# Optimization experiments

Measured on AMD Instinct MI355X. Metric: run time of the kernel, lower is better.

The kernel has to match this reference:

```python
import jax, jax.numpy as jnp
import numpy as np

N0, D, H, E0 = 50000, 128, 128, 800000
N1, E1, A, B, C = 20000, 320000, 100000, 64, 10


def _gcn(x, row, col, ew, n, W, b):
    # GCNConv: out = D^-1/2 (A + I) D^-1/2 (x W) + b, with edge weights
    xw = x @ W
    sl = jnp.arange(n)
    r = jnp.concatenate([row, sl])
    c = jnp.concatenate([col, sl])
    w = jnp.concatenate([ew, jnp.ones((n,), ew.dtype)])
    deg = jax.ops.segment_sum(w, c, num_segments=n)
    dinv = jax.lax.rsqrt(jnp.maximum(deg, 1e-12))
    norm = dinv[r] * w * dinv[c]
    return jax.ops.segment_sum(norm[:, None] * xw[r], c, num_segments=n) + b


def _block(x, row, col, ew, n, W1, b1, W2, b2, Wl, bl):
    # Block with num_inner_layers=2, jumping_knowledge='cat'
    x1 = jax.nn.relu(_gcn(x, row, col, ew, n, W1, b1))
    x2 = jax.nn.relu(_gcn(x1, row, col, ew, n, W2, b2))
    return jnp.concatenate([x1, x2], axis=1) @ Wl + bl


def _seg_max(x, idx, n):
    m = jax.ops.segment_max(x, idx, num_segments=n)
    return jnp.where(jnp.isfinite(m), m, 0.0)  # empty segments -> 0 like scatter_max default


def _lin_init(k, i, o):
    s = 1.0 / np.sqrt(i)
    return jax.random.uniform(k, (i, o), jnp.float32, -s, s)


def setup_inputs() -> dict:
    key = jax.random.key(0)
    ks = jax.random.split(key, 20)
    x = jax.random.normal(ks[0], (N0, D), jnp.float32)
    edge_index0 = jax.random.randint(ks[1], (2, E0), 0, N0)
    edge_weight0 = jax.random.uniform(ks[2], (E0,), jnp.float32)
    batch0 = jnp.sort(jax.random.randint(ks[3], (N0,), 0, B))
    cover_row = jax.random.randint(ks[4], (A,), 0, N0)
    cover_col = jnp.concatenate([jnp.arange(N1), jax.random.randint(ks[5], (A - N1,), 0, N1)])
    edge_index1 = jax.random.randint(ks[6], (2, E1), 0, N1)
    edge_weight1 = jax.random.uniform(ks[7], (E1,), jnp.float32)
    batch1 = jnp.sort(jax.random.randint(ks[8], (N1,), 0, B))
    params = dict(
        w_in1=_lin_init(ks[9], D, H), b_in1=jnp.zeros((H,), jnp.float32),
        w_in2=_lin_init(ks[10], H, H), b_in2=jnp.zeros((H,), jnp.float32),
        w_in_lin=_lin_init(ks[11], 2 * H, H), b_in_lin=jnp.zeros((H,), jnp.float32),
        w_b1=_lin_init(ks[12], 2 * H, H), b_b1=jnp.zeros((H,), jnp.float32),
        w_b2=_lin_init(ks[13], H, H), b_b2=jnp.zeros((H,), jnp.float32),
        w_b_lin=_lin_init(ks[14], 2 * H, H), b_b_lin=jnp.zeros((H,), jnp.float32),
        bn_gamma=jnp.ones((4 * H,), jnp.float32), bn_beta=jnp.zeros((4 * H,), jnp.float32),
        w_l1=_lin_init(ks[15], 4 * H, H), b_l1=jnp.zeros((H,), jnp.float32),
        w_l2=_lin_init(ks[16], H, C), b_l2=jnp.zeros((C,), jnp.float32),
    )
    return dict(x=x, edge_index0=edge_index0, edge_weight0=edge_weight0, batch0=batch0,
                cover_row=cover_row, cover_col=cover_col, edge_index1=edge_index1,
                edge_weight1=edge_weight1, batch1=batch1, **params)


def reference(x, edge_index0, edge_weight0, batch0, cover_row, cover_col,
              edge_index1, edge_weight1, batch1,
              w_in1, b_in1, w_in2, b_in2, w_in_lin, b_in_lin,
              w_b1, b_b1, w_b2, b_b2, w_b_lin, b_b_lin,
              bn_gamma, bn_beta, w_l1, b_l1, w_l2, b_l2):
    r0, c0 = edge_index0[0], edge_index0[1]
    h = jax.nn.relu(_block(x, r0, c0, edge_weight0, N0, w_in1, b_in1, w_in2, b_in2, w_in_lin, b_in_lin))
    xs = [jax.ops.segment_sum(h, batch0, num_segments=B), _seg_max(h, batch0, B)]
    # cover_pool_node: add + max over k-plex cover assignments
    hg = h[cover_row]
    h2 = jnp.concatenate([jax.ops.segment_sum(hg, cover_col, num_segments=N1),
                          _seg_max(hg, cover_col, N1)], axis=1)
    r1, c1 = edge_index1[0], edge_index1[1]
    h2 = jax.nn.relu(_block(h2, r1, c1, edge_weight1, N1, w_b1, b_b1, w_b2, b_b2, w_b_lin, b_b_lin))
    xs.append(jax.ops.segment_sum(h2, batch1, num_segments=B))
    xs.append(_seg_max(h2, batch1, B))
    z = jnp.concatenate(xs, axis=1)  # [B, 4H]
    # BatchNorm1d in eval mode: running stats (mean=0, var=1), eps=1e-5
    z = z * (bn_gamma * jax.lax.rsqrt(jnp.asarray(1.0 + 1e-5, z.dtype))) + bn_beta
    z = jax.nn.relu(z @ w_l1 + b_l1)
    logits = z @ w_l2 + b_l2  # dropout skipped (eval mode)
    return jax.nn.softmax(logits, axis=-1)
```

## Files before the change

kernel.cpp:

```cpp
#include <hip/hip_runtime.h>
#include <cmath>

#define HF 128
#define EPB 2048

namespace {

typedef __attribute__((ext_vector_type(8))) short short8;
typedef __attribute__((ext_vector_type(4))) float f32x4;

inline int cdiv(int a, int b) { return (a + b - 1) / b; }

__device__ inline unsigned short f2bf(float x) {
    unsigned u = __float_as_uint(x);
    return (unsigned short)((u + 0x7fffu + ((u >> 16) & 1u)) >> 16);
}
__device__ inline float bf2f(unsigned short u) {
    return __uint_as_float((unsigned)u << 16);
}
__device__ inline float bflo(unsigned v) { return __uint_as_float(v << 16); }
__device__ inline float bfhi(unsigned v) { return __uint_as_float(v & 0xffff0000u); }

#define FIXS 4194304.0f
#define FIXINV 2.384185791015625e-07f
#define SUMMASK ((1ULL << 40) - 1)

template <int K, bool AF32>
__device__ __forceinline__ void gemm_dev(int bid, const void* __restrict__ A1v, int lda1,
                                         const void* __restrict__ A2v, int lda2,
                                         const unsigned short* __restrict__ wpk,
                                         const float* __restrict__ bias, int relu,
                                         unsigned short* __restrict__ out, int N) {
    const int t = threadIdx.x;
    const int wv = t >> 6, lane = t & 63;
    const int l15 = lane & 15, lhi = lane >> 4;
    const int rbase = bid * 128 + wv * 32;

    f32x4 acc[2][8];
#pragma unroll
    for (int i = 0; i < 2; ++i)
#pragma unroll
        for (int g = 0; g < 8; ++g) acc[i][g] = {0.f, 0.f, 0.f, 0.f};

    int r[2];
#pragma unroll
    for (int ri = 0; ri < 2; ++ri) {
        int rr = rbase + ri * 16 + l15;
        r[ri] = (rr < N) ? rr : (N - 1);
    }

    for (int kc = 0; kc < K / 32; ++kc) {
        int kb = kc * 32 + lhi * 8;
        short8 a[2];
#pragma unroll
        for (int ri = 0; ri < 2; ++ri) {
            if (AF32) {
                const float* A = (const float*)A1v;
                const float* p = A + (size_t)r[ri] * lda1 + kb;
                float4 f0 = *reinterpret_cast<const float4*>(p);
                float4 f1 = *reinterpret_cast<const float4*>(p + 4);
                a[ri][0] = (short)f2bf(f0.x); a[ri][1] = (short)f2bf(f0.y);
                a[ri][2] = (short)f2bf(f0.z); a[ri][3] = (short)f2bf(f0.w);
                a[ri][4] = (short)f2bf(f1.x); a[ri][5] = (short)f2bf(f1.y);
                a[ri][6] = (short)f2bf(f1.z); a[ri][7] = (short)f2bf(f1.w);
            } else {
                const unsigned short* base;
                int kk, ld;
                if (K == 256 && kb >= 128) { base = (const unsigned short*)A2v; kk = kb - 128; ld = lda2; }
                else                       { base = (const unsigned short*)A1v; kk = kb;       ld = lda1; }
                a[ri] = *reinterpret_cast<const short8*>(base + (size_t)r[ri] * ld + kk);
            }
        }
        const unsigned short* wb = wpk + (size_t)(kc * 8) * 512 + lane * 8;
#pragma unroll
        for (int g = 0; g < 8; ++g) {
            short8 b = *reinterpret_cast<const short8*>(wb + (size_t)g * 512);
            acc[0][g] = __builtin_amdgcn_mfma_f32_16x16x32_bf16(a[0], b, acc[0][g], 0, 0, 0);
            acc[1][g] = __builtin_amdgcn_mfma_f32_16x16x32_bf16(a[1], b, acc[1][g], 0, 0, 0);
        }
    }

#pragma unroll
    for (int ri = 0; ri < 2; ++ri) {
#pragma unroll
        for (int g = 0; g < 8; ++g) {
            int col = l15 + g * 16;
            float bb = bias ? bias[col] : 0.f;
#pragma unroll
            for (int e = 0; e < 4; ++e) {
                int rr = rbase + ri * 16 + lhi * 4 + e;
                if (rr < N) {
                    float v = acc[ri][g][e] + bb;
                    if (relu) v = fmaxf(v, 0.f);
                    out[(size_t)rr * 128 + col] = f2bf(v);
                }
            }
        }
    }
}

template <int K, bool AF32>
__global__ void k_mfma_gemm(const void* __restrict__ A1v, int lda1,
                            const void* __restrict__ A2v, int lda2,
                            const unsigned short* __restrict__ wpk,
                            const float* __restrict__ bias, int relu,
                            unsigned short* __restrict__ out, int N) {
    gemm_dev<K, AF32>(blockIdx.x, A1v, lda1, A2v, lda2, wpk, bias, relu, out, N);
}

__device__ __forceinline__ void hist_dev(int e, int E, const int* __restrict__ col,
                                         const float* __restrict__ ew,
                                         unsigned long long* __restrict__ dc,
                                         unsigned* __restrict__ rank) {
    if (e < E) {
        unsigned long long v = (1ULL << 40) | (unsigned long long)(ew[e] * FIXS + 0.5f);
        unsigned long long old = atomicAdd(&dc[col[e]], v);
        rank[e] = (unsigned)(old >> 40);
    }
}

__device__ inline void scan256(int* s, int v, int gid, int n, int* __restrict__ excl,
                               int* __restrict__ partial, int pb) {
    s[threadIdx.x] = v;
    __syncthreads();
    for (int off = 1; off < 256; off <<= 1) {
        int t = (threadIdx.x >= off) ? s[threadIdx.x - off] : 0;
        __syncthreads();
        s[threadIdx.x] += t;
        __syncthreads();
    }
    if (gid < n) excl[gid] = s[threadIdx.x] - v;
    if (threadIdx.x == 255) partial[pb] = s[255];
}

__device__ __forceinline__ void fill_dev(int b, int t, const int* __restrict__ row,
                                         const int* __restrict__ col, const float* __restrict__ ew,
                                         const unsigned* __restrict__ rank,
                                         const float* __restrict__ dinv, const int* __restrict__ rp,
                                         int2* __restrict__ ed, int E, int Nn) {
    int xcd = b & 7, chunk = b >> 3;
    int lo = (int)((long long)Nn * xcd >> 3), hi = (int)((long long)Nn * (xcd + 1) >> 3);
    int base = chunk * EPB;
#pragma unroll
    for (int i = 0; i < EPB; i += 256) {
        int e = base + i + t;
        if (e < E) {
            int c = col[e];
            if (c >= lo && c < hi) {
                int r = row[e];
                ed[rp[c] + rank[e]] = make_int2(r, __float_as_int(ew[e] * dinv[r] * dinv[c]));
            }
        }
    }
}

__device__ __forceinline__ void gather_dev(int b, const unsigned* __restrict__ xw, int n,
                                           const int* __restrict__ rp, const int2* __restrict__ ed,
                                           const float* __restrict__ dinv,
                                           const float* __restrict__ bias,
                                           unsigned* __restrict__ out) {
    int wid = (b * 256 + (int)threadIdx.x) >> 6;
    if (wid >= n) return;
    int lane = threadIdx.x & 63;
    int s = rp[wid], e = rp[wid + 1];
    float d = dinv[wid];
    unsigned v = xw[(size_t)wid * 64 + lane];
    float ax = bflo(v) * d * d, ay = bfhi(v) * d * d;
    float bx = 0.f, by = 0.f, cx = 0.f, cy = 0.f, dx = 0.f, dy = 0.f;
    int i = s;
    for (; i + 4 <= e; i += 4) {
        unsigned long long p0 = __builtin_nontemporal_load((const unsigned long long*)(ed + i));
        unsigned long long p1 = __builtin_nontemporal_load((const unsigned long long*)(ed + i + 1));
        unsigned long long p2 = __builtin_nontemporal_load((const unsigned long long*)(ed + i + 2));
        unsigned long long p3 = __builtin_nontemporal_load((const unsigned long long*)(ed + i + 3));
        unsigned v0 = xw[(size_t)(unsigned)(p0 & 0xffffffffu) * 64 + lane];
        unsigned v1 = xw[(size_t)(unsigned)(p1 & 0xffffffffu) * 64 + lane];
        unsigned v2 = xw[(size_t)(unsigned)(p2 & 0xffffffffu) * 64 + lane];
        unsigned v3 = xw[(size_t)(unsigned)(p3 & 0xffffffffu) * 64 + lane];
        float c0 = __uint_as_float((unsigned)(p0 >> 32));
        float c1 = __uint_as_float((unsigned)(p1 >> 32));
        float c2 = __uint_as_float((unsigned)(p2 >> 32));
        float c3 = __uint_as_float((unsigned)(p3 >> 32));
        ax += c0 * bflo(v0); ay += c0 * bfhi(v0);
        bx += c1 * bflo(v1); by += c1 * bfhi(v1);
        cx += c2 * bflo(v2); cy += c2 * bfhi(v2);
        dx += c3 * bflo(v3); dy += c3 * bfhi(v3);
    }
    for (; i < e; ++i) {
        unsigned long long p0 = __builtin_nontemporal_load((const unsigned long long*)(ed + i));
        unsigned v0 = xw[(size_t)(unsigned)(p0 & 0xffffffffu) * 64 + lane];
        float c0 = __uint_as_float((unsigned)(p0 >> 32));
        ax += c0 * bflo(v0); ay += c0 * bfhi(v0);
    }
    ax += bx + cx + dx;
    ay += by + cy + dy;
    float2 bb = *reinterpret_cast<const float2*>(bias + lane * 2);
    ax = fmaxf(ax + bb.x, 0.f);
    ay = fmaxf(ay + bb.y, 0.f);
    out[(size_t)wid * 64 + lane] = (unsigned)f2bf(ax) | ((unsigned)f2bf(ay) << 16);
}

__global__ void k_prep0(const float* __restrict__ w0, const float* __restrict__ w1,
                        const float* __restrict__ w2, const float* __restrict__ w3,
                        const float* __restrict__ w4, const float* __restrict__ w5,
                        unsigned short* __restrict__ wpk,
                        const int* __restrict__ b0, int n0, const int* __restrict__ b1,
                        int n1, int B, int* __restrict__ bst0, int* __restrict__ bst1) {
    int b = blockIdx.x, t = threadIdx.x;
    if (b < 576) {
        int idx = b * 256 + t;
        const float* src; int local;
        if      (idx < 16384)  { src = w0; local = idx; }
        else if (idx < 32768)  { src = w1; local = idx - 16384; }
        else if (idx < 65536)  { src = w2; local = idx - 32768; }
        else if (idx < 98304)  { src = w3; local = idx - 65536; }
        else if (idx < 114688) { src = w4; local = idx - 98304; }
        else                   { src = w5; local = idx - 114688; }
        int e = local & 7, lane = (local >> 3) & 63, g = (local >> 9) & 7, kc = local >> 12;
        int colw = (lane & 15) + 16 * g;
        int k = kc * 32 + ((lane >> 4) << 3) + e;
        wpk[idx] = f2bf(src[k * 128 + colw]);
        return;
    }
    int idx = t;
    if (idx < 2 * (B + 1)) {
        int which = idx > B;
        int bb = which ? idx - (B + 1) : idx;
        const int* arr = which ? b1 : b0;
        int lo = 0, hi = which ? n1 : n0;
        while (lo < hi) {
            int mid = (lo + hi) >> 1;
            if (arr[mid] < bb) lo = mid + 1; else hi = mid;
        }
        (which ? bst1 : bst0)[bb] = lo;
    }
}

__global__ void k_prep1(const float* __restrict__ x, const unsigned short* __restrict__ wpk,
                        unsigned short* __restrict__ xw, int N0gemm, int nbG,
                        const int* __restrict__ col0, const float* __restrict__ ew0,
                        unsigned long long* __restrict__ dc0, unsigned* __restrict__ rank0,
                        int E0) {
    int b = blockIdx.x;
    if (b < nbG) {
        gemm_dev<128, true>(b, x, 128, nullptr, 0, wpk, nullptr, 0, xw, N0gemm);
        return;
    }
    b -= nbG;
    hist_dev(b * 256 + (int)threadIdx.x, E0, col0, ew0, dc0, rank0);
}

__global__ void k_scanA(const unsigned long long* __restrict__ dc0, int* __restrict__ rp0,
                        int* __restrict__ part0, float* __restrict__ dinv0, int n0) {
    __shared__ int s[256];
    int gid = blockIdx.x * 256 + threadIdx.x;
    int v = (gid < n0) ? (int)(dc0[gid] >> 40) : 0;
    scan256(s, v, gid, n0, rp0, part0, blockIdx.x);
    if (gid < n0) dinv0[gid] = rsqrtf(1.0f + (float)(dc0[gid] & SUMMASK) * FIXINV);
}

__global__ void k_scan2a(int* __restrict__ p0, int nb0) {
    __shared__ int s[256];
    int v = (threadIdx.x < nb0) ? p0[threadIdx.x] : 0;
    s[threadIdx.x] = v;
    __syncthreads();
    for (int off = 1; off < 256; off <<= 1) {
        int t = (threadIdx.x >= off) ? s[threadIdx.x - off] : 0;
        __syncthreads();
        s[threadIdx.x] += t;
        __syncthreads();
    }
    if (threadIdx.x < nb0) p0[threadIdx.x] = s[threadIdx.x] - v;
}

__global__ void k_scan3a(int* __restrict__ rp0, const int* __restrict__ part0, int n0, int tot) {
    int gid = blockIdx.x * 256 + threadIdx.x;
    if (gid < n0) rp0[gid] += part0[blockIdx.x];
    if (gid == 0) rp0[n0] = tot;
}

__global__ void k_fill0(const int* __restrict__ row0, const int* __restrict__ col0,
                        const float* __restrict__ ew0, const unsigned* __restrict__ rank0,
                        const float* __restrict__ dinv0, const int* __restrict__ rp0,
                        int2* __restrict__ ed0, int E0, int N0n) {
    fill_dev(blockIdx.x, threadIdx.x, row0, col0, ew0, rank0, dinv0, rp0, ed0, E0, N0n);
}

__global__ void k_gather_hist(const unsigned* __restrict__ xw, int n,
                              const int* __restrict__ rp, const int2* __restrict__ ed,
                              const float* __restrict__ dinv, const float* __restrict__ bias,
                              unsigned* __restrict__ out, int G,
                              const int* __restrict__ col1, const float* __restrict__ ew1,
                              unsigned long long* __restrict__ dc1, unsigned* __restrict__ rank1,
                              int E1, int nb1,
                              const int* __restrict__ ccol, int* __restrict__ ccnt,
                              unsigned* __restrict__ rankc, int A) {
    int b = blockIdx.x;
    if (b < G) { gather_dev(b, xw, n, rp, ed, dinv, bias, out); return; }
    b -= G;
    int t = threadIdx.x;
    if (b < nb1) { hist_dev(b * 256 + t, E1, col1, ew1, dc1, rank1); return; }
    b -= nb1;
    int e = b * 256 + t;
    if (e < A) rankc[e] = (unsigned)atomicAdd(&ccnt[ccol[e]], 1);
}

__global__ void k_gemm_scan(const void* __restrict__ A1v, const unsigned short* __restrict__ wpk,
                            unsigned short* __restrict__ out, int N, int nbG,
                            const unsigned long long* __restrict__ dc1, int* __restrict__ rp1,
                            int* __restrict__ part1, float* __restrict__ dinv1, int n1, int nbs1,
                            const int* __restrict__ ccnt, int* __restrict__ crp,
                            int* __restrict__ cpart, int nc) {
    __shared__ int s[256];
    int b = blockIdx.x;
    if (b < nbG) {
        gemm_dev<128, false>(b, A1v, 128, nullptr, 0, wpk, nullptr, 0, out, N);
        return;
    }
    b -= nbG;
    if (b < nbs1) {
        int gid = b * 256 + threadIdx.x;
        int v = (gid < n1) ? (int)(dc1[gid] >> 40) : 0;
        scan256(s, v, gid, n1, rp1, part1, b);
        if (gid < n1) dinv1[gid] = rsqrtf(1.0f + (float)(dc1[gid] & SUMMASK) * FIXINV);
        return;
    }
    b -= nbs1;
    {
        int gid = b * 256 + threadIdx.x;
        int v = (gid < nc) ? ccnt[gid] : 0;
        scan256(s, v, gid, nc, crp, cpart, b);
    }
}

__global__ void k_scan2b(int* __restrict__ p1, int nb1, int* __restrict__ p2, int nb2) {
    __shared__ int s[256];
    int* p = (blockIdx.x == 0) ? p1 : p2;
    int nb = (blockIdx.x == 0) ? nb1 : nb2;
    int v = (threadIdx.x < nb) ? p[threadIdx.x] : 0;
    s[threadIdx.x] = v;
    __syncthreads();
    for (int off = 1; off < 256; off <<= 1) {
        int t = (threadIdx.x >= off) ? s[threadIdx.x - off] : 0;
        __syncthreads();
        s[threadIdx.x] += t;
        __syncthreads();
    }
    if (threadIdx.x < nb) p[threadIdx.x] = s[threadIdx.x] - v;
}

__global__ void k_scan3b(int* __restrict__ rp1, const int* __restrict__ part1, int n1, int tot1,
                         int nb1, int* __restrict__ crp, const int* __restrict__ cpart,
                         int nc, int totc) {
    int b = blockIdx.x, t = threadIdx.x;
    if (b < nb1) {
        int gid = b * 256 + t;
        if (gid < n1) rp1[gid] += part1[b];
        if (gid == 0) rp1[n1] = tot1;
        return;
    }
    b -= nb1;
    int gid = b * 256 + t;
    if (gid < nc) crp[gid] += cpart[b];
    if (gid == 0) crp[nc] = totc;
}

__global__ void k_gather_fill(const unsigned* __restrict__ xw, int n,
                              const int* __restrict__ rp, const int2* __restrict__ ed,
                              const float* __restrict__ dinv, const float* __restrict__ bias,
                              unsigned* __restrict__ out, int G,
                              const int* __restrict__ row1, const int* __restrict__ col1,
                              const float* __restrict__ ew1, const unsigned* __restrict__ rank1,
                              const float* __restrict__ dinv1, const int* __restrict__ rp1,
                              int2* __restrict__ ed1, int E1, int N1n, int g1b,
                              const int* __restrict__ crow, const int* __restrict__ ccol,
                              const unsigned* __restrict__ rankc, const int* __restrict__ crp,
                              int* __restrict__ csrcs, int A) {
    int b = blockIdx.x, t = threadIdx.x;
    if (b < G) { gather_dev(b, xw, n, rp, ed, dinv, bias, out); return; }
    b -= G;
    if (b < g1b) { fill_dev(b, t, row1, col1, ew1, rank1, dinv1, rp1, ed1, E1, N1n); return; }
    b -= g1b;
    {
        int xcd = b & 7, chunk = b >> 3;
        int lo = (int)((long long)N1n * xcd >> 3), hi = (int)((long long)N1n * (xcd + 1) >> 3);
        int base = chunk * EPB;
#pragma unroll
        for (int i = 0; i < EPB; i += 256) {
            int e = base + i + t;
            if (e < A) {
                int c = ccol[e];
                if (c >= lo && c < hi) csrcs[crp[c] + rankc[e]] = crow[e];
            }
        }
    }
}

__global__ void k_gather(const unsigned* __restrict__ xw, int n, const int* __restrict__ rp,
                         const int2* __restrict__ ed, const float* __restrict__ dinv,
                         const float* __restrict__ bias, unsigned* __restrict__ out) {
    gather_dev(blockIdx.x, xw, n, rp, ed, dinv, bias, out);
}

__global__ void k_pool_cover(const unsigned short* __restrict__ h, const int* __restrict__ bst,
                             float* __restrict__ psum, float* __restrict__ pmax, int nsplit,
                             int nbpool, const unsigned* __restrict__ h32,
                             const int* __restrict__ crp, const int* __restrict__ csrcs,
                             unsigned* __restrict__ h2, int n1) {
    int t = threadIdx.x;
    if ((int)blockIdx.x < nbpool) {
        int blk = blockIdx.x;
        int b = blk / nsplit, sub = (blk % nsplit) * 2 + (t >> 7);
        int col = t & 127;
        int r0 = bst[b], r1 = bst[b + 1];
        float sum = 0.f, mx = 0.f;
        for (int r = r0 + sub; r < r1; r += 2 * nsplit) {
            float v = bf2f(h[(size_t)r * HF + col]);
            sum += v;
            mx = fmaxf(mx, v);
        }
        atomicAdd(&psum[b * HF + col], sum);
        atomicMax(reinterpret_cast<int*>(&pmax[b * HF + col]), __float_as_int(mx));
        return;
    }
    int wid = (((int)blockIdx.x - nbpool) * 256 + t) >> 6;
    if (wid >= n1) return;
    int lane = t & 63;
    int s = crp[wid], e = crp[wid + 1];
    float sx = 0.f, sy = 0.f, mx = 0.f, my = 0.f;
    for (int i = s; i < e; ++i) {
        unsigned v = h32[(size_t)csrcs[i] * 64 + lane];
        float vx = bflo(v), vy = bfhi(v);
        sx += vx; sy += vy;
        mx = fmaxf(mx, vx); my = fmaxf(my, vy);
    }
    h2[(size_t)wid * 128 + lane]      = (unsigned)f2bf(sx) | ((unsigned)f2bf(sy) << 16);
    h2[(size_t)wid * 128 + 64 + lane] = (unsigned)f2bf(mx) | ((unsigned)f2bf(my) << 16);
}

__global__ void k_pool256(const unsigned short* __restrict__ h, const int* __restrict__ bst,
                          float* __restrict__ psum, float* __restrict__ pmax, int nsplit) {
    int t = threadIdx.x;
    int blk = blockIdx.x;
    int b = blk / nsplit, sub = (blk % nsplit) * 2 + (t >> 7);
    int col = t & 127;
    int r0 = bst[b], r1 = bst[b + 1];
    float sum = 0.f, mx = 0.f;
    for (int r = r0 + sub; r < r1; r += 2 * nsplit) {
        float v = bf2f(h[(size_t)r * HF + col]);
        sum += v;
        mx = fmaxf(mx, v);
    }
    atomicAdd(&psum[b * HF + col], sum);
    atomicMax(reinterpret_cast<int*>(&pmax[b * HF + col]), __float_as_int(mx));
}

__global__ void k_head(const float* __restrict__ p0s, const float* __restrict__ p0m,
                       const float* __restrict__ p1s, const float* __restrict__ p1m,
                       const float* __restrict__ gamma, const float* __restrict__ beta,
                       const float* __restrict__ w1, const float* __restrict__ b1,
                       const float* __restrict__ w2, const float* __restrict__ b2,
                       float* __restrict__ out) {
    __shared__ float z[512];
    __shared__ float z1[128];
    __shared__ float lg[10];
    int b = blockIdx.x, t = threadIdx.x;
    const float s = rsqrtf(1.0f + 1e-5f);
    z[t]       = p0s[b * 128 + t] * (gamma[t] * s)       + beta[t];
    z[128 + t] = p0m[b * 128 + t] * (gamma[128 + t] * s) + beta[128 + t];
    z[256 + t] = p1s[b * 128 + t] * (gamma[256 + t] * s) + beta[256 + t];
    z[384 + t] = p1m[b * 128 + t] * (gamma[384 + t] * s) + beta[384 + t];
    __syncthreads();
    float acc = b1[t];
    for (int k = 0; k < 512; ++k) acc += z[k] * w1[k * 128 + t];
    z1[t] = fmaxf(acc, 0.f);
    __syncthreads();
    if (t < 10) {
        float a2 = b2[t];
        for (int k = 0; k < 128; ++k) a2 += z1[k] * w2[k * 10 + t];
        lg[t] = a2;
    }
    __syncthreads();
    if (t == 0) {
        float m = lg[0];
        for (int c = 1; c < 10; ++c) m = fmaxf(m, lg[c]);
        float e[10], ssum = 0.f;
        for (int c = 0; c < 10; ++c) { e[c] = expf(lg[c] - m); ssum += e[c]; }
        for (int c = 0; c < 10; ++c) out[b * 10 + c] = e[c] / ssum;
    }
}

}

extern "C" void kernel_launch(void* const* d_in, const int* in_sizes, int n_in,
                              void* d_out, int out_size, void* d_ws, size_t ws_size,
                              hipStream_t stream) {
    const float* x      = (const float*)d_in[0];
    const int*   ei0    = (const int*)d_in[1];
    const float* ew0    = (const float*)d_in[2];
    const int*   batch0 = (const int*)d_in[3];
    const int*   crow   = (const int*)d_in[4];
    const int*   ccol   = (const int*)d_in[5];
    const int*   ei1    = (const int*)d_in[6];
    const float* ew1    = (const float*)d_in[7];
    const int*   batch1 = (const int*)d_in[8];
    const float* w_in1  = (const float*)d_in[9];
    const float* b_in1  = (const float*)d_in[10];
    const float* w_in2  = (const float*)d_in[11];
    const float* b_in2  = (const float*)d_in[12];
    const float* w_inl  = (const float*)d_in[13];
    const float* b_inl  = (const float*)d_in[14];
    const float* w_b1   = (const float*)d_in[15];
    const float* b_b1   = (const float*)d_in[16];
    const float* w_b2   = (const float*)d_in[17];
    const float* b_b2   = (const float*)d_in[18];
    const float* w_bl   = (const float*)d_in[19];
    const float* b_bl   = (const float*)d_in[20];
    const float* gamma  = (const float*)d_in[21];
    const float* beta   = (const float*)d_in[22];
    const float* w_l1   = (const float*)d_in[23];
    const float* b_l1   = (const float*)d_in[24];
    const float* w_l2   = (const float*)d_in[25];
    const float* b_l2   = (const float*)d_in[26];

    const int N0 = in_sizes[0] / 128;
    const int E0 = in_sizes[2];
    const int A  = in_sizes[4];
    const int E1 = in_sizes[7];
    const int N1 = in_sizes[8];
    const int B  = out_size / 10;

    const int* row0 = ei0;
    const int* col0 = ei0 + E0;
    const int* row1 = ei1;
    const int* col1 = ei1 + E1;

    char* wsp = (char*)d_ws;
    size_t off = 0;
    auto alloc = [&](size_t bytes) -> char* {
        char* p = wsp + off;
        off += (bytes + 255) & ~(size_t)255;
        return p;
    };
    unsigned long long* dc0 = (unsigned long long*)alloc((size_t)N0 * 8);
    unsigned long long* dc1 = (unsigned long long*)alloc((size_t)N1 * 8);
    int*   ccnt  = (int*)alloc((size_t)N1 * 4);
    float* p0s   = (float*)alloc((size_t)B * HF * 4 * 4);
    float* p0m   = p0s + (size_t)B * HF;
    float* p1s   = p0m + (size_t)B * HF;
    float* p1m   = p1s + (size_t)B * HF;
    size_t zero_bytes = off;

    unsigned* xw  = (unsigned*)alloc((size_t)N0 * 64 * 4);
    unsigned* x1  = (unsigned*)alloc((size_t)N0 * 64 * 4);
    unsigned* x2  = (unsigned*)alloc((size_t)N0 * 64 * 4);
    unsigned* h   = (unsigned*)alloc((size_t)N0 * 64 * 4);
    unsigned* h2  = (unsigned*)alloc((size_t)N1 * 128 * 4);
    unsigned short* wpk = (unsigned short*)alloc(147456 * 2);
    float* dinv0 = (float*)alloc((size_t)N0 * 4);
    float* dinv1 = (float*)alloc((size_t)N1 * 4);
    int*   rp0   = (int*)alloc(((size_t)N0 + 1) * 4);
    int*   rp1   = (int*)alloc(((size_t)N1 + 1) * 4);
    int*   crp   = (int*)alloc(((size_t)N1 + 1) * 4);
    int*   part0 = (int*)alloc(256 * 4);
    int*   part1 = (int*)alloc(256 * 4);
    int*   cpart = (int*)alloc(256 * 4);
    int2*  ed0   = (int2*)alloc((size_t)E0 * 8);
    int2*  ed1   = (int2*)alloc((size_t)E1 * 8);
    int*   csrcs = (int*)alloc((size_t)A * 4);
    unsigned* rank0 = (unsigned*)alloc((size_t)E0 * 4);
    unsigned* rank1 = (unsigned*)alloc((size_t)E1 * 4);
    unsigned* rankc = (unsigned*)alloc((size_t)A * 4);
    int*   bst0  = (int*)alloc((size_t)(B + 1) * 4);
    int*   bst1  = (int*)alloc((size_t)(B + 1) * 4);
    (void)ws_size; (void)n_in;

    const int NSPLIT = 16;
    const int nbG0 = cdiv(N0, 128), nbG1 = cdiv(N1, 128);
    const int nbE0 = cdiv(E0, 256), nbE1 = cdiv(E1, 256), nbC = cdiv(A, 256);
    const int nbs0 = cdiv(N0, 256), nbs1 = cdiv(N1, 256), nbsc = cdiv(N1, 256);
    const int g1f = cdiv(E1, EPB) * 8, gcf = cdiv(A, EPB) * 8, g0f = cdiv(E0, EPB) * 8;
    const int G0 = cdiv(N0, 4), G1 = cdiv(N1, 4);

    hipMemsetAsync(dc0, 0, zero_bytes, stream);

    k_prep0<<<577, 256, 0, stream>>>(w_in1, w_in2, w_inl, w_b1, w_b2, w_bl, wpk,
                                     batch0, N0, batch1, N1, B, bst0, bst1);

    k_prep1<<<nbG0 + nbE0, 256, 0, stream>>>(x, wpk, (unsigned short*)xw, N0, nbG0,
                                             col0, ew0, dc0, rank0, E0);

    k_scanA<<<nbs0, 256, 0, stream>>>(dc0, rp0, part0, dinv0, N0);
    k_scan2a<<<1, 256, 0, stream>>>(part0, nbs0);
    k_scan3a<<<nbs0, 256, 0, stream>>>(rp0, part0, N0, E0);
    k_fill0<<<g0f, 256, 0, stream>>>(row0, col0, ew0, rank0, dinv0, rp0, ed0, E0, N0);

    k_gather_hist<<<G0 + nbE1 + nbC, 256, 0, stream>>>(
        xw, N0, rp0, ed0, dinv0, b_in1, x1, G0,
        col1, ew1, dc1, rank1, E1, nbE1, ccol, ccnt, rankc, A);

    k_gemm_scan<<<nbG0 + nbs1 + nbsc, 256, 0, stream>>>(
        x1, wpk + 16384, (unsigned short*)xw, N0, nbG0,
        dc1, rp1, part1, dinv1, N1, nbs1, ccnt, crp, cpart, N1);

    k_scan2b<<<2, 256, 0, stream>>>(part1, nbs1, cpart, nbsc);
    k_scan3b<<<nbs1 + nbsc, 256, 0, stream>>>(rp1, part1, N1, E1, nbs1, crp, cpart, N1, A);

    k_gather_fill<<<G0 + g1f + gcf, 256, 0, stream>>>(
        xw, N0, rp0, ed0, dinv0, b_in2, x2, G0,
        row1, col1, ew1, rank1, dinv1, rp1, ed1, E1, N1, g1f,
        crow, ccol, rankc, crp, csrcs, A);

    k_mfma_gemm<256, false><<<nbG0, 256, 0, stream>>>(
        x1, 128, (const unsigned short*)x2, 128, wpk + 32768, b_inl, 1,
        (unsigned short*)h, N0);

    k_pool_cover<<<B * NSPLIT + cdiv(N1, 4), 256, 0, stream>>>(
        (const unsigned short*)h, bst0, p0s, p0m, NSPLIT, B * NSPLIT,
        h, crp, csrcs, h2, N1);

    k_mfma_gemm<256, false><<<nbG1, 256, 0, stream>>>(
        h2, 256, (const unsigned short*)h2 + 128, 256, wpk + 65536, nullptr, 0,
        (unsigned short*)xw, N1);
    k_gather<<<G1, 256, 0, stream>>>(xw, N1, rp1, ed1, dinv1, b_b1, x1);
    k_mfma_gemm<128, false><<<nbG1, 256, 0, stream>>>(
        x1, 128, nullptr, 0, wpk + 98304, nullptr, 0, (unsigned short*)xw, N1);
    k_gather<<<G1, 256, 0, stream>>>(xw, N1, rp1, ed1, dinv1, b_b2, x2);
    k_mfma_gemm<256, false><<<nbG1, 256, 0, stream>>>(
        x1, 128, (const unsigned short*)x2, 128, wpk + 114688, b_bl, 1,
        (unsigned short*)h, N1);

    k_pool256<<<B * NSPLIT, 256, 0, stream>>>((const unsigned short*)h, bst1, p1s, p1m, NSPLIT);

    k_head<<<B, 128, 0, stream>>>(p0s, p0m, p1s, p1m, gamma, beta, w_l1, b_l1, w_l2, b_l2,
                                  (float*)d_out);
}
```

Measured before the change: 397.6 us.

## Bucket CSR edges by source-row chunk to improve gather locality

Splits each destination node's CSR segment into sub-buckets keyed by the source row's 8192-node chunk, so edges within each row are ordered by source region and gathered feature rows are more clustered in cache. The histogram, scans (now 8 elements per thread) and fill use the composite key, and dinv is computed by summing across sub-buckets. The gather loop also switches from nontemporal 8-byte loads to aligned 16-byte edge loads with an alignment prologue. The cost is larger count and offset arrays, more scan work, and extra memset bytes.

```diff
diff --git a/kernel.cpp b/kernel.cpp
--- a/kernel.cpp
+++ b/kernel.cpp
@@ -3,11 +3,13 @@
 
 #define HF 128
 #define EPB 2048
+#define CSH 13
 
 namespace {
 
 typedef __attribute__((ext_vector_type(8))) short short8;
 typedef __attribute__((ext_vector_type(4))) float f32x4;
+typedef unsigned long long u64;
 
 inline int cdiv(int a, int b) { return (a + b - 1) / b; }
 
@@ -108,36 +110,45 @@
     gemm_dev<K, AF32>(blockIdx.x, A1v, lda1, A2v, lda2, wpk, bias, relu, out, N);
 }
 
-__device__ __forceinline__ void hist_dev(int e, int E, const int* __restrict__ col,
-                                         const float* __restrict__ ew,
-                                         unsigned long long* __restrict__ dc,
-                                         unsigned* __restrict__ rank) {
+__device__ __forceinline__ void hist_dev(int e, int E, const int* __restrict__ row,
+                                         const int* __restrict__ col,
+                                         const float* __restrict__ ew, int NC,
+                                         u64* __restrict__ dc, unsigned* __restrict__ rank) {
     if (e < E) {
-        unsigned long long v = (1ULL << 40) | (unsigned long long)(ew[e] * FIXS + 0.5f);
-        unsigned long long old = atomicAdd(&dc[col[e]], v);
+        int key = col[e] * NC + (row[e] >> CSH);
+        u64 v = (1ULL << 40) | (u64)(ew[e] * FIXS + 0.5f);
+        u64 old = atomicAdd(&dc[key], v);
         rank[e] = (unsigned)(old >> 40);
     }
 }
 
-__device__ inline void scan256(int* s, int v, int gid, int n, int* __restrict__ excl,
-                               int* __restrict__ partial, int pb) {
-    s[threadIdx.x] = v;
+__device__ __forceinline__ void scanBig(int* s, const int* v8, int tsum, int b, int n2,
+                                        int* __restrict__ rp, int* __restrict__ part) {
+    int t = threadIdx.x;
+    s[t] = tsum;
     __syncthreads();
     for (int off = 1; off < 256; off <<= 1) {
-        int t = (threadIdx.x >= off) ? s[threadIdx.x - off] : 0;
+        int tv = (t >= off) ? s[t - off] : 0;
         __syncthreads();
-        s[threadIdx.x] += t;
+        s[t] += tv;
         __syncthreads();
     }
-    if (gid < n) excl[gid] = s[threadIdx.x] - v;
-    if (threadIdx.x == 255) partial[pb] = s[255];
+    int excl = s[t] - tsum;
+    int g0 = b * 2048 + t * 8;
+#pragma unroll
+    for (int j = 0; j < 8; ++j) {
+        int g = g0 + j;
+        if (g < n2) rp[g] = excl;
+        excl += v8[j];
+    }
+    if (t == 255) part[b] = s[255];
 }
 
 __device__ __forceinline__ void fill_dev(int b, int t, const int* __restrict__ row,
                                          const int* __restrict__ col, const float* __restrict__ ew,
                                          const unsigned* __restrict__ rank,
-                                         const float* __restrict__ dinv, const int* __restrict__ rp,
-                                         int2* __restrict__ ed, int E, int Nn) {
+                                         const float* __restrict__ dinv, const int* __restrict__ rp2,
+                                         int NC, int2* __restrict__ ed, int E, int Nn) {
     int xcd = b & 7, chunk = b >> 3;
     int lo = (int)((long long)Nn * xcd >> 3), hi = (int)((long long)Nn * (xcd + 1) >> 3);
     int base = chunk * EPB;
@@ -148,48 +159,52 @@
             int c = col[e];
             if (c >= lo && c < hi) {
                 int r = row[e];
-                ed[rp[c] + rank[e]] = make_int2(r, __float_as_int(ew[e] * dinv[r] * dinv[c]));
+                int key = c * NC + (r >> CSH);
+                ed[rp2[key] + rank[e]] = make_int2(r, __float_as_int(ew[e] * dinv[r] * dinv[c]));
             }
         }
     }
 }
 
-__device__ __forceinline__ void gather_dev(int b, const unsigned* __restrict__ xw, int n,
-                                           const int* __restrict__ rp, const int2* __restrict__ ed,
+__device__ __forceinline__ void gather_dev(int b, const unsigned* __restrict__ xw, int n, int NC,
+                                           const int* __restrict__ rp2, const int2* __restrict__ ed,
                                            const float* __restrict__ dinv,
                                            const float* __restrict__ bias,
                                            unsigned* __restrict__ out) {
     int wid = (b * 256 + (int)threadIdx.x) >> 6;
     if (wid >= n) return;
     int lane = threadIdx.x & 63;
-    int s = rp[wid], e = rp[wid + 1];
+    int s = rp2[(size_t)wid * NC], e = rp2[(size_t)wid * NC + NC];
     float d = dinv[wid];
     unsigned v = xw[(size_t)wid * 64 + lane];
     float ax = bflo(v) * d * d, ay = bfhi(v) * d * d;
     float bx = 0.f, by = 0.f, cx = 0.f, cy = 0.f, dx = 0.f, dy = 0.f;
     int i = s;
+    if ((i & 1) && i < e) {
+        int2 e0 = ed[i];
+        unsigned v0 = xw[(size_t)e0.x * 64 + lane];
+        float c0 = __int_as_float(e0.y);
+        ax += c0 * bflo(v0); ay += c0 * bfhi(v0);
+        ++i;
+    }
     for (; i + 4 <= e; i += 4) {
-        unsigned long long p0 = __builtin_nontemporal_load((const unsigned long long*)(ed + i));
-        unsigned long long p1 = __builtin_nontemporal_load((const unsigned long long*)(ed + i + 1));
-        unsigned long long p2 = __builtin_nontemporal_load((const unsigned long long*)(ed + i + 2));
-        unsigned long long p3 = __builtin_nontemporal_load((const unsigned long long*)(ed + i + 3));
-        unsigned v0 = xw[(size_t)(unsigned)(p0 & 0xffffffffu) * 64 + lane];
-        unsigned v1 = xw[(size_t)(unsigned)(p1 & 0xffffffffu) * 64 + lane];
-        unsigned v2 = xw[(size_t)(unsigned)(p2 & 0xffffffffu) * 64 + lane];
-        unsigned v3 = xw[(size_t)(unsigned)(p3 & 0xffffffffu) * 64 + lane];
-        float c0 = __uint_as_float((unsigned)(p0 >> 32));
-        float c1 = __uint_as_float((unsigned)(p1 >> 32));
-        float c2 = __uint_as_float((unsigned)(p2 >> 32));
-        float c3 = __uint_as_float((unsigned)(p3 >> 32));
+        int4 q0 = *reinterpret_cast<const int4*>(ed + i);
+        int4 q1 = *reinterpret_cast<const int4*>(ed + i + 2);
+        unsigned v0 = xw[(size_t)q0.x * 64 + lane];
+        unsigned v1 = xw[(size_t)q0.z * 64 + lane];
+        unsigned v2 = xw[(size_t)q1.x * 64 + lane];
+        unsigned v3 = xw[(size_t)q1.z * 64 + lane];
+        float c0 = __int_as_float(q0.y), c1 = __int_as_float(q0.w);
+        float c2 = __int_as_float(q1.y), c3 = __int_as_float(q1.w);
         ax += c0 * bflo(v0); ay += c0 * bfhi(v0);
         bx += c1 * bflo(v1); by += c1 * bfhi(v1);
         cx += c2 * bflo(v2); cy += c2 * bfhi(v2);
         dx += c3 * bflo(v3); dy += c3 * bfhi(v3);
     }
     for (; i < e; ++i) {
-        unsigned long long p0 = __builtin_nontemporal_load((const unsigned long long*)(ed + i));
-        unsigned v0 = xw[(size_t)(unsigned)(p0 & 0xffffffffu) * 64 + lane];
-        float c0 = __uint_as_float((unsigned)(p0 >> 32));
+        int2 e0 = ed[i];
+        unsigned v0 = xw[(size_t)e0.x * 64 + lane];
+        float c0 = __int_as_float(e0.y);
         ax += c0 * bflo(v0); ay += c0 * bfhi(v0);
     }
     ax += bx + cx + dx;
@@ -238,25 +253,41 @@
 
 __global__ void k_prep1(const float* __restrict__ x, const unsigned short* __restrict__ wpk,
                         unsigned short* __restrict__ xw, int N0gemm, int nbG,
-                        const int* __restrict__ col0, const float* __restrict__ ew0,
-                        unsigned long long* __restrict__ dc0, unsigned* __restrict__ rank0,
-                        int E0) {
+                        const int* __restrict__ row0, const int* __restrict__ col0,
+                        const float* __restrict__ ew0, int NC0,
+                        u64* __restrict__ dc0, unsigned* __restrict__ rank0, int E0) {
     int b = blockIdx.x;
     if (b < nbG) {
         gemm_dev<128, true>(b, x, 128, nullptr, 0, wpk, nullptr, 0, xw, N0gemm);
         return;
     }
     b -= nbG;
-    hist_dev(b * 256 + (int)threadIdx.x, E0, col0, ew0, dc0, rank0);
-}
-
-__global__ void k_scanA(const unsigned long long* __restrict__ dc0, int* __restrict__ rp0,
-                        int* __restrict__ part0, float* __restrict__ dinv0, int n0) {
+    hist_dev(b * 256 + (int)threadIdx.x, E0, row0, col0, ew0, NC0, dc0, rank0);
+}
+
+__global__ void k_scanA(const u64* __restrict__ dc0, int* __restrict__ rp2, int* __restrict__ part,
+                        float* __restrict__ dinv0, int n2, int nbs, int NC, int n0) {
     __shared__ int s[256];
-    int gid = blockIdx.x * 256 + threadIdx.x;
-    int v = (gid < n0) ? (int)(dc0[gid] >> 40) : 0;
-    scan256(s, v, gid, n0, rp0, part0, blockIdx.x);
-    if (gid < n0) dinv0[gid] = rsqrtf(1.0f + (float)(dc0[gid] & SUMMASK) * FIXINV);
+    int b = blockIdx.x, t = threadIdx.x;
+    if (b < nbs) {
+        int g0 = b * 2048 + t * 8;
+        int v8[8]; int tsum = 0;
+#pragma unroll
+        for (int j = 0; j < 8; ++j) {
+            int g = g0 + j;
+            v8[j] = (g < n2) ? (int)(dc0[g] >> 40) : 0;
+            tsum += v8[j];
+        }
+        scanBig(s, v8, tsum, b, n2, rp2, part);
+        return;
+    }
+    b -= nbs;
+    int i = b * 256 + t;
+    if (i < n0) {
+        u64 acc = 0;
+        for (int c = 0; c < NC; ++c) acc += dc0[(size_t)i * NC + c] & SUMMASK;
+        dinv0[i] = rsqrtf(1.0f + (float)acc * FIXINV);
+    }
 }
 
 __global__ void k_scan2a(int* __restrict__ p0, int nb0) {
@@ -273,63 +304,96 @@
     if (threadIdx.x < nb0) p0[threadIdx.x] = s[threadIdx.x] - v;
 }
 
-__global__ void k_scan3a(int* __restrict__ rp0, const int* __restrict__ part0, int n0, int tot) {
-    int gid = blockIdx.x * 256 + threadIdx.x;
-    if (gid < n0) rp0[gid] += part0[blockIdx.x];
-    if (gid == 0) rp0[n0] = tot;
+__global__ void k_scan3a(int* __restrict__ rp2, const int* __restrict__ part, int n2, int tot) {
+    int b = blockIdx.x, t = threadIdx.x;
+    int g0 = b * 2048 + t * 8;
+    int p = part[b];
+#pragma unroll
+    for (int j = 0; j < 8; ++j) {
+        int g = g0 + j;
+        if (g < n2) rp2[g] += p;
+    }
+    if (g0 == 0) rp2[n2] = tot;
 }
 
 __global__ void k_fill0(const int* __restrict__ row0, const int* __restrict__ col0,
                         const float* __restrict__ ew0, const unsigned* __restrict__ rank0,
-                        const float* __restrict__ dinv0, const int* __restrict__ rp0,
+                        const float* __restrict__ dinv0, const int* __restrict__ rp2, int NC0,
                         int2* __restrict__ ed0, int E0, int N0n) {
-    fill_dev(blockIdx.x, threadIdx.x, row0, col0, ew0, rank0, dinv0, rp0, ed0, E0, N0n);
-}
-
-__global__ void k_gather_hist(const unsigned* __restrict__ xw, int n,
-                              const int* __restrict__ rp, const int2* __restrict__ ed,
+    fill_dev(blockIdx.x, threadIdx.x, row0, col0, ew0, rank0, dinv0, rp2, NC0, ed0, E0, N0n);
+}
+
+__global__ void k_gather_hist(const unsigned* __restrict__ xw, int n, int NC,
+                              const int* __restrict__ rp2, const int2* __restrict__ ed,
                               const float* __restrict__ dinv, const float* __restrict__ bias,
                               unsigned* __restrict__ out, int G,
-                              const int* __restrict__ col1, const float* __restrict__ ew1,
-                              unsigned long long* __restrict__ dc1, unsigned* __restrict__ rank1,
+                              const int* __restrict__ row1, const int* __restrict__ col1,
+                              const float* __restrict__ ew1, int NC1,
+                              u64* __restrict__ dc1, unsigned* __restrict__ rank1,
                               int E1, int nb1,
-                              const int* __restrict__ ccol, int* __restrict__ ccnt,
-                              unsigned* __restrict__ rankc, int A) {
+                              const int* __restrict__ crow, const int* __restrict__ ccol,
+                              int NCC, int* __restrict__ ccnt2, unsigned* __restrict__ rankc,
+                              int A) {
     int b = blockIdx.x;
-    if (b < G) { gather_dev(b, xw, n, rp, ed, dinv, bias, out); return; }
+    if (b < G) { gather_dev(b, xw, n, NC, rp2, ed, dinv, bias, out); return; }
     b -= G;
     int t = threadIdx.x;
-    if (b < nb1) { hist_dev(b * 256 + t, E1, col1, ew1, dc1, rank1); return; }
+    if (b < nb1) { hist_dev(b * 256 + t, E1, row1, col1, ew1, NC1, dc1, rank1); return; }
     b -= nb1;
     int e = b * 256 + t;
-    if (e < A) rankc[e] = (unsigned)atomicAdd(&ccnt[ccol[e]], 1);
+    if (e < A) {
+        int key = ccol[e] * NCC + (crow[e] >> CSH);
+        rankc[e] = (unsigned)atomicAdd(&ccnt2[key], 1);
+    }
 }
 
 __global__ void k_gemm_scan(const void* __restrict__ A1v, const unsigned short* __restrict__ wpk,
                             unsigned short* __restrict__ out, int N, int nbG,
-                            const unsigned long long* __restrict__ dc1, int* __restrict__ rp1,
-                            int* __restrict__ part1, float* __restrict__ dinv1, int n1, int nbs1,
-                            const int* __restrict__ ccnt, int* __restrict__ crp,
-                            int* __restrict__ cpart, int nc) {
+                            const u64* __restrict__ dc1, int* __restrict__ rp1,
+                            int* __restrict__ part1, int n21, int nbs1,
+                            float* __restrict__ dinv1, int NC1, int n1, int nbd1,
+                            const int* __restrict__ ccnt2, int* __restrict__ crp2,
+                            int* __restrict__ cpart, int n2c) {
     __shared__ int s[256];
-    int b = blockIdx.x;
+    int b = blockIdx.x, t = threadIdx.x;
     if (b < nbG) {
         gemm_dev<128, false>(b, A1v, 128, nullptr, 0, wpk, nullptr, 0, out, N);
         return;
     }
     b -= nbG;
     if (b < nbs1) {
-        int gid = b * 256 + threadIdx.x;
-        int v = (gid < n1) ? (int)(dc1[gid] >> 40) : 0;
-        scan256(s, v, gid, n1, rp1, part1, b);
-        if (gid < n1) dinv1[gid] = rsqrtf(1.0f + (float)(dc1[gid] & SUMMASK) * FIXINV);
+        int g0 = b * 2048 + t * 8;
+        int v8[8]; int tsum = 0;
+#pragma unroll
+        for (int j = 0; j < 8; ++j) {
+            int g = g0 + j;
+            v8[j] = (g < n21) ? (int)(dc1[g] >> 40) : 0;
+            tsum += v8[j];
+        }
+        scanBig(s, v8, tsum, b, n21, rp1, part1);
         return;
     }
     b -= nbs1;
+    if (b < nbd1) {
+        int i = b * 256 + t;
+        if (i < n1) {
+            u64 acc = 0;
+            for (int c = 0; c < NC1; ++c) acc += dc1[(size_t)i * NC1 + c] & SUMMASK;
+            dinv1[i] = rsqrtf(1.0f + (float)acc * FIXINV);
+        }
+        return;
+    }
+    b -= nbd1;
     {
-        int gid = b * 256 + threadIdx.x;
-        int v = (gid < nc) ? ccnt[gid] : 0;
-        scan256(s, v, gid, nc, crp, cpart, b);
+        int g0 = b * 2048 + t * 8;
+        int v8[8]; int tsum = 0;
+#pragma unroll
+        for (int j = 0; j < 8; ++j) {
+            int g = g0 + j;
+            v8[j] = (g < n2c) ? ccnt2[g] : 0;
+            tsum += v8[j];
+        }
+        scanBig(s, v8, tsum, b, n2c, crp2, cpart);
     }
 }
 
@@ -349,37 +413,52 @@
     if (threadIdx.x < nb) p[threadIdx.x] = s[threadIdx.x] - v;
 }
 
-__global__ void k_scan3b(int* __restrict__ rp1, const int* __restrict__ part1, int n1, int tot1,
-                         int nb1, int* __restrict__ crp, const int* __restrict__ cpart,
-                         int nc, int totc) {
+__global__ void k_scan3b(int* __restrict__ rp1, const int* __restrict__ part1, int n21, int tot1,
+                         int nb1, int* __restrict__ crp2, const int* __restrict__ cpart,
+                         int n2c, int totc) {
     int b = blockIdx.x, t = threadIdx.x;
     if (b < nb1) {
-        int gid = b * 256 + t;
-        if (gid < n1) rp1[gid] += part1[b];
-        if (gid == 0) rp1[n1] = tot1;
+        int g0 = b * 2048 + t * 8;
+        int p = part1[b];
+#pragma unroll
+        for (int j = 0; j < 8; ++j) {
+            int g = g0 + j;
+            if (g < n21) rp1[g] += p;
+        }
+        if (g0 == 0) rp1[n21] = tot1;
         return;
     }
     b -= nb1;
-    int gid = b * 256 + t;
-    if (gid < nc) crp[gid] += cpart[b];
-    if (gid == 0) crp[nc] = totc;
-}
-
-__global__ void k_gather_fill(const unsigned* __restrict__ xw, int n,
-                              const int* __restrict__ rp, const int2* __restrict__ ed,
+    {
+        int g0 = b * 2048 + t * 8;
+        int p = cpart[b];
+#pragma unroll
+        for (int j = 0; j < 8; ++j) {
+            int g = g0 + j;
+            if (g < n2c) crp2[g] += p;
+        }
+        if (g0 == 0) crp2[n2c] = totc;
+    }
+}
+
+__global__ void k_gather_fill(const unsigned* __restrict__ xw, int n, int NC,
+                              const int* __restrict__ rp2, const int2* __restrict__ ed,
                               const float* __restrict__ dinv, const float* __restrict__ bias,
                               unsigned* __restrict__ out, int G,
                               const int* __restrict__ row1, const int* __restrict__ col1,
                               const float* __restrict__ ew1, const unsigned* __restrict__ rank1,
                               const float* __restrict__ dinv1, const int* __restrict__ rp1,
-                              int2* __restrict__ ed1, int E1, int N1n, int g1b,
+                              int NC1, int2* __restrict__ ed1, int E1, int N1n, int g1b,
                               const int* __restrict__ crow, const int* __restrict__ ccol,
-                              const unsigned* __restrict__ rankc, const int* __restrict__ crp,
-                              int* __restrict__ csrcs, int A) {
+                              const unsigned* __restrict__ rankc, const int* __restrict__ crp2,
+                              int NCC, int* __restrict__ csrcs, int A) {
     int b = blockIdx.x, t = threadIdx.x;
-    if (b < G) { gather_dev(b, xw, n, rp, ed, dinv, bias, out); return; }
+    if (b < G) { gather_dev(b, xw, n, NC, rp2, ed, dinv, bias, out); return; }
     b -= G;
-    if (b < g1b) { fill_dev(b, t, row1, col1, ew1, rank1, dinv1, rp1, ed1, E1, N1n); return; }
+    if (b < g1b) {
+        fill_dev(b, t, row1, col1, ew1, rank1, dinv1, rp1, NC1, ed1, E1, N1n);
+        return;
+    }
     b -= g1b;
     {
         int xcd = b & 7, chunk = b >> 3;
@@ -390,23 +469,27 @@
             int e = base + i + t;
             if (e < A) {
                 int c = ccol[e];
-                if (c >= lo && c < hi) csrcs[crp[c] + rankc[e]] = crow[e];
+                if (c >= lo && c < hi) {
+                    int r = crow[e];
+                    csrcs[crp2[c * NCC + (r >> CSH)] + rankc[e]] = r;
+                }
             }
         }
     }
 }
 
-__global__ void k_gather(const unsigned* __restrict__ xw, int n, const int* __restrict__ rp,
-                         const int2* __restrict__ ed, const float* __restrict__ dinv,
-                         const float* __restrict__ bias, unsigned* __restrict__ out) {
-    gather_dev(blockIdx.x, xw, n, rp, ed, dinv, bias, out);
+__global__ void k_gather(const unsigned* __restrict__ xw, int n, int NC,
+                         const int* __restrict__ rp2, const int2* __restrict__ ed,
+                         const float* __restrict__ dinv, const float* __restrict__ bias,
+                         unsigned* __restrict__ out) {
+    gather_dev(blockIdx.x, xw, n, NC, rp2, ed, dinv, bias, out);
 }
 
 __global__ void k_pool_cover(const unsigned short* __restrict__ h, const int* __restrict__ bst,
                              float* __restrict__ psum, float* __restrict__ pmax, int nsplit,
                              int nbpool, const unsigned* __restrict__ h32,
-                             const int* __restrict__ crp, const int* __restrict__ csrcs,
-                             unsigned* __restrict__ h2, int n1) {
+                             const int* __restrict__ crp2, int NCC,
+                             const int* __restrict__ csrcs, unsigned* __restrict__ h2, int n1) {
     int t = threadIdx.x;
     if ((int)blockIdx.x < nbpool) {
         int blk = blockIdx.x;
@@ -426,7 +509,7 @@
     int wid = (((int)blockIdx.x - nbpool) * 256 + t) >> 6;
     if (wid >= n1) return;
     int lane = t & 63;
-    int s = crp[wid], e = crp[wid + 1];
+    int s = crp2[(size_t)wid * NCC], e = crp2[(size_t)wid * NCC + NCC];
     float sx = 0.f, sy = 0.f, mx = 0.f, my = 0.f;
     for (int i = s; i < e; ++i) {
         unsigned v = h32[(size_t)csrcs[i] * 64 + lane];
@@ -535,6 +618,11 @@
     const int* row1 = ei1;
     const int* col1 = ei1 + E1;
 
+    const int NC0 = cdiv(N0, 1 << CSH);
+    const int NC1 = cdiv(N1, 1 << CSH);
+    const int NCC = NC0;
+    const int n2_0 = N0 * NC0, n2_1 = N1 * NC1, n2_c = N1 * NCC;
+
     char* wsp = (char*)d_ws;
     size_t off = 0;
     auto alloc = [&](size_t bytes) -> char* {
@@ -542,13 +630,13 @@
         off += (bytes + 255) & ~(size_t)255;
         return p;
     };
-    unsigned long long* dc0 = (unsigned long long*)alloc((size_t)N0 * 8);
-    unsigned long long* dc1 = (unsigned long long*)alloc((size_t)N1 * 8);
-    int*   ccnt  = (int*)alloc((size_t)N1 * 4);
-    float* p0s   = (float*)alloc((size_t)B * HF * 4 * 4);
-    float* p0m   = p0s + (size_t)B * HF;
-    float* p1s   = p0m + (size_t)B * HF;
-    float* p1m   = p1s + (size_t)B * HF;
+    u64*  dc0   = (u64*)alloc((size_t)n2_0 * 8);
+    u64*  dc1   = (u64*)alloc((size_t)n2_1 * 8);
+    int*  ccnt2 = (int*)alloc((size_t)n2_c * 4);
+    float* p0s  = (float*)alloc((size_t)B * HF * 4 * 4);
+    float* p0m  = p0s + (size_t)B * HF;
+    float* p1s  = p0m + (size_t)B * HF;
+    float* p1m  = p1s + (size_t)B * HF;
     size_t zero_bytes = off;
 
     unsigned* xw  = (unsigned*)alloc((size_t)N0 * 64 * 4);
@@ -559,9 +647,9 @@
     unsigned short* wpk = (unsigned short*)alloc(147456 * 2);
     float* dinv0 = (float*)alloc((size_t)N0 * 4);
     float* dinv1 = (float*)alloc((size_t)N1 * 4);
-    int*   rp0   = (int*)alloc(((size_t)N0 + 1) * 4);
-    int*   rp1   = (int*)alloc(((size_t)N1 + 1) * 4);
-    int*   crp   = (int*)alloc(((size_t)N1 + 1) * 4);
+    int*   rp0   = (int*)alloc(((size_t)n2_0 + 1) * 4);
+    int*   rp1   = (int*)alloc(((size_t)n2_1 + 1) * 4);
+    int*   crp2  = (int*)alloc(((size_t)n2_c + 1) * 4);
     int*   part0 = (int*)alloc(256 * 4);
     int*   part1 = (int*)alloc(256 * 4);
     int*   cpart = (int*)alloc(256 * 4);
@@ -578,8 +666,9 @@
     const int NSPLIT = 16;
     const int nbG0 = cdiv(N0, 128), nbG1 = cdiv(N1, 128);
     const int nbE0 = cdiv(E0, 256), nbE1 = cdiv(E1, 256), nbC = cdiv(A, 256);
-    const int nbs0 = cdiv(N0, 256), nbs1 = cdiv(N1, 256), nbsc = cdiv(N1, 256);
-    const int g1f = cdiv(E1, EPB) * 8, gcf = cdiv(A, EPB) * 8, g0f = cdiv(E0, EPB) * 8;
+    const int nbs0 = cdiv(n2_0, 2048), nbs1 = cdiv(n2_1, 2048), nbsc = cdiv(n2_c, 2048);
+    const int nbd0 = cdiv(N0, 256), nbd1 = cdiv(N1, 256);
+    const int g0f = cdiv(E0, EPB) * 8, g1f = cdiv(E1, EPB) * 8, gcf = cdiv(A, EPB) * 8;
     const int G0 = cdiv(N0, 4), G1 = cdiv(N1, 4);
 
     hipMemsetAsync(dc0, 0, zero_bytes, stream);
@@ -588,28 +677,30 @@
                                      batch0, N0, batch1, N1, B, bst0, bst1);
 
     k_prep1<<<nbG0 + nbE0, 256, 0, stream>>>(x, wpk, (unsigned short*)xw, N0, nbG0,
-                                             col0, ew0, dc0, rank0, E0);
-
-    k_scanA<<<nbs0, 256, 0, stream>>>(dc0, rp0, part0, dinv0, N0);
+                                             row0, col0, ew0, NC0, dc0, rank0, E0);
+
+    k_scanA<<<nbs0 + nbd0, 256, 0, stream>>>(dc0, rp0, part0, dinv0, n2_0, nbs0, NC0, N0);
     k_scan2a<<<1, 256, 0, stream>>>(part0, nbs0);
-    k_scan3a<<<nbs0, 256, 0, stream>>>(rp0, part0, N0, E0);
-    k_fill0<<<g0f, 256, 0, stream>>>(row0, col0, ew0, rank0, dinv0, rp0, ed0, E0, N0);
+    k_scan3a<<<nbs0, 256, 0, stream>>>(rp0, part0, n2_0, E0);
+    k_fill0<<<g0f, 256, 0, stream>>>(row0, col0, ew0, rank0, dinv0, rp0, NC0, ed0, E0, N0);
 
     k_gather_hist<<<G0 + nbE1 + nbC, 256, 0, stream>>>(
-        xw, N0, rp0, ed0, dinv0, b_in1, x1, G0,
-        col1, ew1, dc1, rank1, E1, nbE1, ccol, ccnt, rankc, A);
-
-    k_gemm_scan<<<nbG0 + nbs1 + nbsc, 256, 0, stream>>>(
+        xw, N0, NC0, rp0, ed0, dinv0, b_in1, x1, G0,
+        row1, col1, ew1, NC1, dc1, rank1, E1, nbE1,
+        crow, ccol, NCC, ccnt2, rankc, A);
+
+    k_gemm_scan<<<nbG0 + nbs1 + nbd1 + nbsc, 256, 0, stream>>>(
         x1, wpk + 16384, (unsigned short*)xw, N0, nbG0,
-        dc1, rp1, part1, dinv1, N1, nbs1, ccnt, crp, cpart, N1);
+        dc1, rp1, part1, n2_1, nbs1, dinv1, NC1, N1, nbd1,
+        ccnt2, crp2, cpart, n2_c);
 
     k_scan2b<<<2, 256, 0, stream>>>(part1, nbs1, cpart, nbsc);
-    k_scan3b<<<nbs1 + nbsc, 256, 0, stream>>>(rp1, part1, N1, E1, nbs1, crp, cpart, N1, A);
+    k_scan3b<<<nbs1 + nbsc, 256, 0, stream>>>(rp1, part1, n2_1, E1, nbs1, crp2, cpart, n2_c, A);
 
     k_gather_fill<<<G0 + g1f + gcf, 256, 0, stream>>>(
-        xw, N0, rp0, ed0, dinv0, b_in2, x2, G0,
-        row1, col1, ew1, rank1, dinv1, rp1, ed1, E1, N1, g1f,
-        crow, ccol, rankc, crp, csrcs, A);
+        xw, N0, NC0, rp0, ed0, dinv0, b_in2, x2, G0,
+        row1, col1, ew1, rank1, dinv1, rp1, NC1, ed1, E1, N1, g1f,
+        crow, ccol, rankc, crp2, NCC, csrcs, A);
 
     k_mfma_gemm<256, false><<<nbG0, 256, 0, stream>>>(
         x1, 128, (const unsigned short*)x2, 128, wpk + 32768, b_inl, 1,
@@ -617,15 +708,15 @@
 
     k_pool_cover<<<B * NSPLIT + cdiv(N1, 4), 256, 0, stream>>>(
         (const unsigned short*)h, bst0, p0s, p0m, NSPLIT, B * NSPLIT,
-        h, crp, csrcs, h2, N1);
+        h, crp2, NCC, csrcs, h2, N1);
 
     k_mfma_gemm<256, false><<<nbG1, 256, 0, stream>>>(
         h2, 256, (const unsigned short*)h2 + 128, 256, wpk + 65536, nullptr, 0,
         (unsigned short*)xw, N1);
-    k_gather<<<G1, 256, 0, stream>>>(xw, N1, rp1, ed1, dinv1, b_b1, x1);
+    k_gather<<<G1, 256, 0, stream>>>(xw, N1, NC1, rp1, ed1, dinv1, b_b1, x1);
     k_mfma_gemm<128, false><<<nbG1, 256, 0, stream>>>(
         x1, 128, nullptr, 0, wpk + 98304, nullptr, 0, (unsigned short*)xw, N1);
-    k_gather<<<G1, 256, 0, stream>>>(xw, N1, rp1, ed1, dinv1, b_b2, x2);
+    k_gather<<<G1, 256, 0, stream>>>(xw, N1, NC1, rp1, ed1, dinv1, b_b2, x2);
     k_mfma_gemm<256, false><<<nbG1, 256, 0, stream>>>(
         x1, 128, (const unsigned short*)x2, 128, wpk + 114688, b_bl, 1,
         (unsigned short*)h, N1);
```

New measurement: 384.0 us. -3.4%, faster.
